# Kernel tuning notes

Hardware: AMD Instinct MI355X
Metric: run time of the kernel (lower is better)

## Reference

```python
import jax, jax.numpy as jnp
import numpy as np

N_NODES = 50000
N_EDGES = 1600000
D_IN = 192   # n_features + n_graphfea
D_HID = 128


def _gcn_conv(x, W, b, src, dst, dhis, n):
    """GCNConv returning two views.
    view1: symmetric-normalized propagation with self-loops (standard GCN).
    view2: raw neighbor sum of transformed features (to be scaled by D_inv outside).
    dhis: deg_hat^{-1/2} per node, deg_hat = in-degree + 1 (self loop).
    """
    h = x @ W + b                                      # [N, hid]
    w = dhis[src] * dhis[dst]                          # [E] edge norm
    view1 = jax.ops.segment_sum(h[src] * w[:, None], dst, num_segments=n)
    view1 = view1 + h * (dhis * dhis)[:, None]         # self-loop term
    view2 = jax.ops.segment_sum(h[src], dst, num_segments=n)
    return view1, view2


def setup_inputs() -> dict:
    key = jax.random.key(0)
    ks = jax.random.split(key, 12)
    x = jax.random.normal(ks[0], (N_NODES, D_IN), dtype=jnp.float32)
    view2 = jax.random.normal(ks[1], (N_NODES, D_IN), dtype=jnp.float32)
    edge_index = jax.random.randint(ks[2], (2, N_EDGES), 0, N_NODES, dtype=jnp.int64)
    D_inv = jax.random.uniform(ks[3], (N_NODES, 1), dtype=jnp.float32)
    def glorot(k, fan_in, fan_out):
        s = jnp.sqrt(jnp.float32(2.0 / (fan_in + fan_out)))
        return jax.random.normal(k, (fan_in, fan_out), dtype=jnp.float32) * s
    W1 = glorot(ks[4], D_IN, D_HID)
    W2 = glorot(ks[5], D_HID, D_HID)
    W3 = glorot(ks[6], D_HID, D_HID)
    W4 = glorot(ks[7], D_IN, D_HID)
    W5 = glorot(ks[8], D_HID, D_HID)
    W6 = glorot(ks[9], D_HID, D_HID)
    z = jnp.zeros((D_HID,), dtype=jnp.float32)
    return {"x": x, "view2": view2, "edge_index": edge_index, "D_inv": D_inv,
            "W1": W1, "b1": z, "W2": W2, "b2": z, "W3": W3, "b3": z,
            "W4": W4, "b4": z, "W5": W5, "b5": z, "W6": W6, "b6": z}


def reference(x, view2, edge_index, D_inv,
              W1, b1, W2, b2, W3, b3, W4, b4, W5, b5, W6, b6):
    n = x.shape[0]
    src, dst = edge_index[0], edge_index[1]
    deg = jax.ops.segment_sum(jnp.ones_like(dst, dtype=x.dtype), dst, num_segments=n)
    dhis = jax.lax.rsqrt(deg + 1.0)                    # deg_hat^{-1/2}
    relu = jax.nn.relu

    x1v1, x1v2 = _gcn_conv(x, W1, b1, src, dst, dhis, n)
    x2v1, x2v2 = _gcn_conv(view2, W4, b4, src, dst, dhis, n)
    x1 = relu(x1v1 + x2v2 * D_inv)
    x2 = relu(x2v1 + x1v2 * D_inv)

    z1v1, z1v2 = _gcn_conv(x1, W2, b2, src, dst, dhis, n)
    z2v1, z2v2 = _gcn_conv(x2, W5, b5, src, dst, dhis, n)
    z1 = relu(z1v1 + z2v2 * D_inv)
    z2 = relu(z2v1 + z1v2 * D_inv)

    v1v1, v1v2 = _gcn_conv(z1, W3, b3, src, dst, dhis, n)
    v2v1, v2v2 = _gcn_conv(z2, W6, b6, src, dst, dhis, n)
    v1 = relu(v1v1 + v2v2 * D_inv)
    v2 = relu(v2v1 + v1v2 * D_inv)

    q = jnp.concatenate([x1, z1, v1], axis=1)          # [N, 3*hid]
    p = jnp.concatenate([x2, z2, v2], axis=1)
    return q, p
```

## Files before the change

kernel.cpp:

```cpp
#include <hip/hip_runtime.h>

#define N_NODES 50000
#define N_EDGES 1600000
#define D_IN 192
#define D_HID 128

#define NSLICE 8
#define SLICE_SZ ((N_NODES + NSLICE - 1) / NSLICE)

typedef __bf16 bf16x8 __attribute__((ext_vector_type(8)));
typedef float f32x4 __attribute__((ext_vector_type(4)));

__device__ __forceinline__ unsigned short f2b(float x) {
    unsigned u = __builtin_bit_cast(unsigned, x);
    u += 0x7FFFu + ((u >> 16) & 1u);
    return (unsigned short)(u >> 16);
}
__device__ __forceinline__ float blo(unsigned u) {
    return __builtin_bit_cast(float, u << 16);
}
__device__ __forceinline__ float bhi(unsigned u) {
    return __builtin_bit_cast(float, u & 0xFFFF0000u);
}


__global__ void hist_kernel(const int* __restrict__ dst, int E,
                            int* __restrict__ cnt, int* __restrict__ rank) {
    int e = blockIdx.x * blockDim.x + threadIdx.x;
    if (e < E) rank[e] = atomicAdd(&cnt[dst[e]], 1);
}

__global__ __launch_bounds__(256) void scanA(const int* __restrict__ cnt,
                                             int* __restrict__ bsum, int n) {
    int i = blockIdx.x * 256 + threadIdx.x;
    int v = (i < n) ? cnt[i] : 0;
#pragma unroll
    for (int off = 32; off > 0; off >>= 1) v += __shfl_down(v, off);
    __shared__ int ws[4];
    if ((threadIdx.x & 63) == 0) ws[threadIdx.x >> 6] = v;
    __syncthreads();
    if (threadIdx.x == 0) bsum[blockIdx.x] = ws[0] + ws[1] + ws[2] + ws[3];
}

__global__ __launch_bounds__(256) void scanB(const int* __restrict__ bsum,
                                             int* __restrict__ boff,
                                             int* __restrict__ row_ptr, int nb, int n) {
    __shared__ int s[256];
    int tid = threadIdx.x;
    int v = (tid < nb) ? bsum[tid] : 0;
    s[tid] = v;
    __syncthreads();
    for (int off = 1; off < 256; off <<= 1) {
        int add = (tid >= off) ? s[tid - off] : 0;
        __syncthreads();
        s[tid] += add;
        __syncthreads();
    }
    if (tid < nb) boff[tid] = (tid > 0) ? s[tid - 1] : 0;
    if (tid == 0) row_ptr[n] = s[255];
}

__global__ __launch_bounds__(256) void scanC(const int* __restrict__ cnt,
                                             const int* __restrict__ boff,
                                             int* __restrict__ row_ptr,
                                             float* __restrict__ dhis, int n) {
    __shared__ int s[256];
    int tid = threadIdx.x;
    int i = blockIdx.x * 256 + tid;
    int c = (i < n) ? cnt[i] : 0;
    s[tid] = c;
    __syncthreads();
    for (int off = 1; off < 256; off <<= 1) {
        int add = (tid >= off) ? s[tid - off] : 0;
        __syncthreads();
        s[tid] += add;
        __syncthreads();
    }
    if (i < n) {
        int pre = boff[blockIdx.x] + s[tid] - c;
        row_ptr[i] = pre;
        dhis[i] = rsqrtf((float)c + 1.0f);
    }
}

__global__ __launch_bounds__(256) void fill_sliced(
        const int* __restrict__ src, const int* __restrict__ dst,
        const int* __restrict__ rank, const int* __restrict__ row_ptr,
        int* __restrict__ esrc, int E, int nchunks) {
    int slice = blockIdx.x & (NSLICE - 1);
    int chunk = blockIdx.x >> 3;
    int lo = slice * SLICE_SZ;
    int hi = lo + SLICE_SZ;
    int per = (E + nchunks - 1) / nchunks;
    int e0 = chunk * per;
    int e1 = min(e0 + per, E);
    for (int e = e0 + threadIdx.x; e < e1; e += 256) {
        int d = dst[e];
        if (d >= lo && d < hi) {
            esrc[row_ptr[d] + rank[e]] = src[e];
        }
    }
}


__global__ void prep_w(const float* __restrict__ W, unsigned short* __restrict__ Wt, int K) {
    int idx = blockIdx.x * 256 + threadIdx.x;
    if (idx < 128 * K) {
        int j = idx / K, k = idx - j * K;
        Wt[idx] = f2b(W[(size_t)k * 128 + j]);
    }
}


__global__ __launch_bounds__(256) void gemm_mfma(
        const float* __restrict__ A, int lda, int K, int Kp,
        const unsigned short* __restrict__ Wt, const float* __restrict__ bias,
        unsigned short* __restrict__ out, int M) {
    __shared__ __align__(16) unsigned short As[64 * 200];

    int tid = threadIdx.x;
    int row0 = blockIdx.x * 64;

    {
        int r = tid >> 2;
        int q = tid & 3;
        int grow = row0 + r;
        int crow = grow < M ? grow : (M - 1);
        int kq = K >> 2;
        const float* ap = A + (size_t)crow * lda + q * kq;
        unsigned short* sp = As + r * Kp + q * kq;
        for (int k = 0; k < kq; k += 4) {
            float4 v = *(const float4*)(ap + k);
            sp[k + 0] = f2b(v.x); sp[k + 1] = f2b(v.y);
            sp[k + 2] = f2b(v.z); sp[k + 3] = f2b(v.w);
        }
    }
    __syncthreads();

    int wave = tid >> 6, lane = tid & 63;
    int m = lane & 15, quad = lane >> 4;

    f32x4 acc[8];
#pragma unroll
    for (int g = 0; g < 8; ++g) acc[g] = (f32x4){0.f, 0.f, 0.f, 0.f};

    int nsteps = K >> 5;
    for (int ks = 0; ks < nsteps; ++ks) {
        int k0 = ks * 32 + quad * 8;
        bf16x8 af = *(const bf16x8*)(As + (wave * 16 + m) * Kp + k0);
#pragma unroll
        for (int g = 0; g < 8; ++g) {
            bf16x8 bfr = *(const bf16x8*)(Wt + (size_t)(g * 16 + m) * K + k0);
            acc[g] = __builtin_amdgcn_mfma_f32_16x16x32_bf16(af, bfr, acc[g], 0, 0, 0);
        }
    }

#pragma unroll
    for (int g = 0; g < 8; ++g) {
        int col = g * 16 + m;
        float bv = bias[col];
#pragma unroll
        for (int r = 0; r < 4; ++r) {
            int grow = row0 + wave * 16 + quad * 4 + r;
            if (grow < M) out[(size_t)grow * 128 + col] = f2b(acc[g][r] + bv);
        }
    }
}


__global__ __launch_bounds__(256) void agg_kernel(
        const unsigned short* __restrict__ h1b, const unsigned short* __restrict__ h2b,
        const int* __restrict__ row_ptr, const int* __restrict__ esrc,
        const float* __restrict__ dhis, const float* __restrict__ D_inv,
        float* __restrict__ out_q, float* __restrict__ out_p, int n) {
    int wave = threadIdx.x >> 6, lane = threadIdx.x & 63;
    int d = blockIdx.x * 4 + wave;
    if (d >= n) return;

    const unsigned* r1 = (const unsigned*)h1b;
    const unsigned* r2 = (const unsigned*)h2b;

    int e0 = row_ptr[d], e1 = row_ptr[d + 1];
    float a1x = 0.f, a1y = 0.f, g1x = 0.f, g1y = 0.f;
    float a2x = 0.f, a2y = 0.f, g2x = 0.f, g2y = 0.f;

    int e = e0;
    for (; e + 4 <= e1; e += 4) {
        int s0 = esrc[e], s1 = esrc[e + 1], s2 = esrc[e + 2], s3 = esrc[e + 3];
        float d0 = dhis[s0], d1 = dhis[s1], d2 = dhis[s2], d3 = dhis[s3];
        unsigned u10 = r1[(size_t)s0 * 64 + lane], u11 = r1[(size_t)s1 * 64 + lane];
        unsigned u12 = r1[(size_t)s2 * 64 + lane], u13 = r1[(size_t)s3 * 64 + lane];
        unsigned u20 = r2[(size_t)s0 * 64 + lane], u21 = r2[(size_t)s1 * 64 + lane];
        unsigned u22 = r2[(size_t)s2 * 64 + lane], u23 = r2[(size_t)s3 * 64 + lane];
        float v;
        v = blo(u10); a1x += v; g1x = fmaf(v, d0, g1x);
        v = bhi(u10); a1y += v; g1y = fmaf(v, d0, g1y);
        v = blo(u11); a1x += v; g1x = fmaf(v, d1, g1x);
        v = bhi(u11); a1y += v; g1y = fmaf(v, d1, g1y);
        v = blo(u12); a1x += v; g1x = fmaf(v, d2, g1x);
        v = bhi(u12); a1y += v; g1y = fmaf(v, d2, g1y);
        v = blo(u13); a1x += v; g1x = fmaf(v, d3, g1x);
        v = bhi(u13); a1y += v; g1y = fmaf(v, d3, g1y);
        v = blo(u20); a2x += v; g2x = fmaf(v, d0, g2x);
        v = bhi(u20); a2y += v; g2y = fmaf(v, d0, g2y);
        v = blo(u21); a2x += v; g2x = fmaf(v, d1, g2x);
        v = bhi(u21); a2y += v; g2y = fmaf(v, d1, g2y);
        v = blo(u22); a2x += v; g2x = fmaf(v, d2, g2x);
        v = bhi(u22); a2y += v; g2y = fmaf(v, d2, g2y);
        v = blo(u23); a2x += v; g2x = fmaf(v, d3, g2x);
        v = bhi(u23); a2y += v; g2y = fmaf(v, d3, g2y);
    }
    for (; e < e1; ++e) {
        int s = esrc[e];
        float ds = dhis[s];
        unsigned u1 = r1[(size_t)s * 64 + lane];
        unsigned u2 = r2[(size_t)s * 64 + lane];
        float v;
        v = blo(u1); a1x += v; g1x = fmaf(v, ds, g1x);
        v = bhi(u1); a1y += v; g1y = fmaf(v, ds, g1y);
        v = blo(u2); a2x += v; g2x = fmaf(v, ds, g2x);
        v = bhi(u2); a2y += v; g2y = fmaf(v, ds, g2y);
    }

    float dh = dhis[d];
    float di = D_inv[d];
    float dh2 = dh * dh;
    unsigned us1 = r1[(size_t)d * 64 + lane];
    unsigned us2 = r2[(size_t)d * 64 + lane];

    float o1x = fmaf(dh, g1x, fmaf(blo(us1), dh2, a2x * di));
    float o1y = fmaf(dh, g1y, fmaf(bhi(us1), dh2, a2y * di));
    float o2x = fmaf(dh, g2x, fmaf(blo(us2), dh2, a1x * di));
    float o2y = fmaf(dh, g2y, fmaf(bhi(us2), dh2, a1y * di));

    float2 oq = make_float2(fmaxf(o1x, 0.f), fmaxf(o1y, 0.f));
    float2 op = make_float2(fmaxf(o2x, 0.f), fmaxf(o2y, 0.f));
    *(float2*)(out_q + (size_t)d * 384 + lane * 2) = oq;
    *(float2*)(out_p + (size_t)d * 384 + lane * 2) = op;
}


extern "C" void kernel_launch(void* const* d_in, const int* in_sizes, int n_in,
                              void* d_out, int out_size, void* d_ws, size_t ws_size,
                              hipStream_t stream) {
    const float* x     = (const float*)d_in[0];
    const float* view2 = (const float*)d_in[1];
    const int*   eidx  = (const int*)d_in[2];
    const float* D_inv = (const float*)d_in[3];
    const float* W1 = (const float*)d_in[4];  const float* b1 = (const float*)d_in[5];
    const float* W2 = (const float*)d_in[6];  const float* b2 = (const float*)d_in[7];
    const float* W3 = (const float*)d_in[8];  const float* b3 = (const float*)d_in[9];
    const float* W4 = (const float*)d_in[10]; const float* b4 = (const float*)d_in[11];
    const float* W5 = (const float*)d_in[12]; const float* b5 = (const float*)d_in[13];
    const float* W6 = (const float*)d_in[14]; const float* b6 = (const float*)d_in[15];

    const int n = N_NODES;
    const int E = N_EDGES;
    const int* src  = eidx;
    const int* dstv = eidx + E;

    char* ws = (char*)d_ws;
    size_t off = 0;
    auto alloc = [&](size_t bytes) -> void* {
        void* p = ws + off;
        off += (bytes + 255) & ~(size_t)255;
        return p;
    };
    int*   cnt     = (int*)alloc((size_t)n * 4);
    int*   row_ptr = (int*)alloc((size_t)(n + 1) * 4);
    float* dhis    = (float*)alloc((size_t)n * 4);
    int*   rank    = (int*)alloc((size_t)E * 4);
    int*   esrc    = (int*)alloc((size_t)E * 4);
    int*   bsum    = (int*)alloc((size_t)256 * 4);
    int*   boff    = (int*)alloc((size_t)256 * 4);
    unsigned short* h1b = (unsigned short*)alloc((size_t)n * 128 * 2);
    unsigned short* h2b = (unsigned short*)alloc((size_t)n * 128 * 2);
    unsigned short* Wt1 = (unsigned short*)alloc((size_t)128 * 192 * 2);
    unsigned short* Wt4 = (unsigned short*)alloc((size_t)128 * 192 * 2);
    unsigned short* Wt2 = (unsigned short*)alloc((size_t)128 * 128 * 2);
    unsigned short* Wt3 = (unsigned short*)alloc((size_t)128 * 128 * 2);
    unsigned short* Wt5 = (unsigned short*)alloc((size_t)128 * 128 * 2);
    unsigned short* Wt6 = (unsigned short*)alloc((size_t)128 * 128 * 2);

    float* qb = (float*)d_out;
    float* pb = qb + (size_t)n * 384;

    hipMemsetAsync(cnt, 0, (size_t)n * 4, stream);
    int eblocks = (E + 255) / 256;
    int nb = (n + 255) / 256;
    hist_kernel<<<eblocks, 256, 0, stream>>>(dstv, E, cnt, rank);
    scanA<<<nb, 256, 0, stream>>>(cnt, bsum, n);
    scanB<<<1, 256, 0, stream>>>(bsum, boff, row_ptr, nb, n);
    scanC<<<nb, 256, 0, stream>>>(cnt, boff, row_ptr, dhis, n);
    int nchunks = 1024;
    fill_sliced<<<nchunks * NSLICE, 256, 0, stream>>>(src, dstv, rank, row_ptr, esrc, E, nchunks);

    prep_w<<<(128 * 192 + 255) / 256, 256, 0, stream>>>(W1, Wt1, 192);
    prep_w<<<(128 * 192 + 255) / 256, 256, 0, stream>>>(W4, Wt4, 192);
    prep_w<<<(128 * 128 + 255) / 256, 256, 0, stream>>>(W2, Wt2, 128);
    prep_w<<<(128 * 128 + 255) / 256, 256, 0, stream>>>(W3, Wt3, 128);
    prep_w<<<(128 * 128 + 255) / 256, 256, 0, stream>>>(W5, Wt5, 128);
    prep_w<<<(128 * 128 + 255) / 256, 256, 0, stream>>>(W6, Wt6, 128);

    int gblocks = (n + 63) / 64;
    int ablocks = (n + 3) / 4;

    gemm_mfma<<<gblocks, 256, 0, stream>>>(x,     D_IN, 192, 200, Wt1, b1, h1b, n);
    gemm_mfma<<<gblocks, 256, 0, stream>>>(view2, D_IN, 192, 200, Wt4, b4, h2b, n);
    agg_kernel<<<ablocks, 256, 0, stream>>>(h1b, h2b, row_ptr, esrc, dhis, D_inv, qb + 0, pb + 0, n);

    gemm_mfma<<<gblocks, 256, 0, stream>>>(qb, 384, 128, 136, Wt2, b2, h1b, n);
    gemm_mfma<<<gblocks, 256, 0, stream>>>(pb, 384, 128, 136, Wt5, b5, h2b, n);
    agg_kernel<<<ablocks, 256, 0, stream>>>(h1b, h2b, row_ptr, esrc, dhis, D_inv, qb + 128, pb + 128, n);

    gemm_mfma<<<gblocks, 256, 0, stream>>>(qb + 128, 384, 128, 136, Wt3, b3, h1b, n);
    gemm_mfma<<<gblocks, 256, 0, stream>>>(pb + 128, 384, 128, 136, Wt6, b6, h2b, n);
    agg_kernel<<<ablocks, 256, 0, stream>>>(h1b, h2b, row_ptr, esrc, dhis, D_inv, qb + 256, pb + 256, n);
}
```

Before: 852.6 us.

## Interleave both views' features and pack edge source with its norm weight

The GEMMs now write both views' bf16 features into one combined row per node, with column pairs interleaved, so the aggregation issues one 8-byte gather per edge instead of two 4-byte gathers. The CSR fill step stores the source index together with dhis[src] as an int2, which removes the dependent dhis gather in the aggregation loop. The aggregation math uses packed float2 vector ops. The GEMM output stores become strided 4-byte-apart scatters, and the edge array doubles in size.

```diff
diff --git a/kernel.cpp b/kernel.cpp
--- a/kernel.cpp
+++ b/kernel.cpp
@@ -10,6 +10,7 @@
 
 typedef __bf16 bf16x8 __attribute__((ext_vector_type(8)));
 typedef float f32x4 __attribute__((ext_vector_type(4)));
+typedef float f32x2 __attribute__((ext_vector_type(2)));
 
 __device__ __forceinline__ unsigned short f2b(float x) {
     unsigned u = __builtin_bit_cast(unsigned, x);
@@ -86,7 +87,8 @@
 __global__ __launch_bounds__(256) void fill_sliced(
         const int* __restrict__ src, const int* __restrict__ dst,
         const int* __restrict__ rank, const int* __restrict__ row_ptr,
-        int* __restrict__ esrc, int E, int nchunks) {
+        const float* __restrict__ dhis,
+        int2* __restrict__ edata, int E, int nchunks) {
     int slice = blockIdx.x & (NSLICE - 1);
     int chunk = blockIdx.x >> 3;
     int lo = slice * SLICE_SZ;
@@ -97,7 +99,9 @@
     for (int e = e0 + threadIdx.x; e < e1; e += 256) {
         int d = dst[e];
         if (d >= lo && d < hi) {
-            esrc[row_ptr[d] + rank[e]] = src[e];
+            int s = src[e];
+            edata[row_ptr[d] + rank[e]] =
+                make_int2(s, __builtin_bit_cast(int, dhis[s]));
         }
     }
 }
@@ -115,7 +119,7 @@
 __global__ __launch_bounds__(256) void gemm_mfma(
         const float* __restrict__ A, int lda, int K, int Kp,
         const unsigned short* __restrict__ Wt, const float* __restrict__ bias,
-        unsigned short* __restrict__ out, int M) {
+        unsigned short* __restrict__ out, int view, int M) {
     __shared__ __align__(16) unsigned short As[64 * 200];
 
     int tid = threadIdx.x;
@@ -159,84 +163,78 @@
     for (int g = 0; g < 8; ++g) {
         int col = g * 16 + m;
         float bv = bias[col];
+        int ci = ((col >> 1) << 2) + (view << 1) + (col & 1);
 #pragma unroll
         for (int r = 0; r < 4; ++r) {
             int grow = row0 + wave * 16 + quad * 4 + r;
-            if (grow < M) out[(size_t)grow * 128 + col] = f2b(acc[g][r] + bv);
+            if (grow < M) out[(size_t)grow * 256 + ci] = f2b(acc[g][r] + bv);
         }
     }
 }
 
 
 __global__ __launch_bounds__(256) void agg_kernel(
-        const unsigned short* __restrict__ h1b, const unsigned short* __restrict__ h2b,
-        const int* __restrict__ row_ptr, const int* __restrict__ esrc,
+        const unsigned* __restrict__ hcomb,
+        const int* __restrict__ row_ptr, const int2* __restrict__ edata,
         const float* __restrict__ dhis, const float* __restrict__ D_inv,
         float* __restrict__ out_q, float* __restrict__ out_p, int n) {
     int wave = threadIdx.x >> 6, lane = threadIdx.x & 63;
     int d = blockIdx.x * 4 + wave;
     if (d >= n) return;
 
-    const unsigned* r1 = (const unsigned*)h1b;
-    const unsigned* r2 = (const unsigned*)h2b;
-
     int e0 = row_ptr[d], e1 = row_ptr[d + 1];
-    float a1x = 0.f, a1y = 0.f, g1x = 0.f, g1y = 0.f;
-    float a2x = 0.f, a2y = 0.f, g2x = 0.f, g2y = 0.f;
+    f32x2 a1 = {0.f, 0.f}, g1 = {0.f, 0.f};
+    f32x2 a2 = {0.f, 0.f}, g2 = {0.f, 0.f};
+
+#define EDGE_BODY(u, w) {                                         \
+        f32x2 v1 = {blo((u).x), bhi((u).x)};                      \
+        f32x2 v2 = {blo((u).y), bhi((u).y)};                      \
+        f32x2 wv = {(w), (w)};                                    \
+        a1 += v1; g1 = __builtin_elementwise_fma(v1, wv, g1);     \
+        a2 += v2; g2 = __builtin_elementwise_fma(v2, wv, g2); }
 
     int e = e0;
     for (; e + 4 <= e1; e += 4) {
-        int s0 = esrc[e], s1 = esrc[e + 1], s2 = esrc[e + 2], s3 = esrc[e + 3];
-        float d0 = dhis[s0], d1 = dhis[s1], d2 = dhis[s2], d3 = dhis[s3];
-        unsigned u10 = r1[(size_t)s0 * 64 + lane], u11 = r1[(size_t)s1 * 64 + lane];
-        unsigned u12 = r1[(size_t)s2 * 64 + lane], u13 = r1[(size_t)s3 * 64 + lane];
-        unsigned u20 = r2[(size_t)s0 * 64 + lane], u21 = r2[(size_t)s1 * 64 + lane];
-        unsigned u22 = r2[(size_t)s2 * 64 + lane], u23 = r2[(size_t)s3 * 64 + lane];
-        float v;
-        v = blo(u10); a1x += v; g1x = fmaf(v, d0, g1x);
-        v = bhi(u10); a1y += v; g1y = fmaf(v, d0, g1y);
-        v = blo(u11); a1x += v; g1x = fmaf(v, d1, g1x);
-        v = bhi(u11); a1y += v; g1y = fmaf(v, d1, g1y);
-        v = blo(u12); a1x += v; g1x = fmaf(v, d2, g1x);
-        v = bhi(u12); a1y += v; g1y = fmaf(v, d2, g1y);
-        v = blo(u13); a1x += v; g1x = fmaf(v, d3, g1x);
-        v = bhi(u13); a1y += v; g1y = fmaf(v, d3, g1y);
-        v = blo(u20); a2x += v; g2x = fmaf(v, d0, g2x);
-        v = bhi(u20); a2y += v; g2y = fmaf(v, d0, g2y);
-        v = blo(u21); a2x += v; g2x = fmaf(v, d1, g2x);
-        v = bhi(u21); a2y += v; g2y = fmaf(v, d1, g2y);
-        v = blo(u22); a2x += v; g2x = fmaf(v, d2, g2x);
-        v = bhi(u22); a2y += v; g2y = fmaf(v, d2, g2y);
-        v = blo(u23); a2x += v; g2x = fmaf(v, d3, g2x);
-        v = bhi(u23); a2y += v; g2y = fmaf(v, d3, g2y);
+        int4 ea = *(const int4*)(edata + e);
+        int4 eb = *(const int4*)(edata + e + 2);
+        uint2 u0 = *((const uint2*)(hcomb + ((size_t)ea.x << 7)) + lane);
+        uint2 u1 = *((const uint2*)(hcomb + ((size_t)ea.z << 7)) + lane);
+        uint2 u2 = *((const uint2*)(hcomb + ((size_t)eb.x << 7)) + lane);
+        uint2 u3 = *((const uint2*)(hcomb + ((size_t)eb.z << 7)) + lane);
+        float w0 = __builtin_bit_cast(float, ea.y);
+        float w1 = __builtin_bit_cast(float, ea.w);
+        float w2 = __builtin_bit_cast(float, eb.y);
+        float w3 = __builtin_bit_cast(float, eb.w);
+        EDGE_BODY(u0, w0); EDGE_BODY(u1, w1);
+        EDGE_BODY(u2, w2); EDGE_BODY(u3, w3);
     }
     for (; e < e1; ++e) {
-        int s = esrc[e];
-        float ds = dhis[s];
-        unsigned u1 = r1[(size_t)s * 64 + lane];
-        unsigned u2 = r2[(size_t)s * 64 + lane];
-        float v;
-        v = blo(u1); a1x += v; g1x = fmaf(v, ds, g1x);
-        v = bhi(u1); a1y += v; g1y = fmaf(v, ds, g1y);
-        v = blo(u2); a2x += v; g2x = fmaf(v, ds, g2x);
-        v = bhi(u2); a2y += v; g2y = fmaf(v, ds, g2y);
-    }
+        int2 ed = edata[e];
+        uint2 u = *((const uint2*)(hcomb + ((size_t)ed.x << 7)) + lane);
+        float w = __builtin_bit_cast(float, ed.y);
+        EDGE_BODY(u, w);
+    }
+#undef EDGE_BODY
 
     float dh = dhis[d];
     float di = D_inv[d];
     float dh2 = dh * dh;
-    unsigned us1 = r1[(size_t)d * 64 + lane];
-    unsigned us2 = r2[(size_t)d * 64 + lane];
-
-    float o1x = fmaf(dh, g1x, fmaf(blo(us1), dh2, a2x * di));
-    float o1y = fmaf(dh, g1y, fmaf(bhi(us1), dh2, a2y * di));
-    float o2x = fmaf(dh, g2x, fmaf(blo(us2), dh2, a1x * di));
-    float o2y = fmaf(dh, g2y, fmaf(bhi(us2), dh2, a1y * di));
-
-    float2 oq = make_float2(fmaxf(o1x, 0.f), fmaxf(o1y, 0.f));
-    float2 op = make_float2(fmaxf(o2x, 0.f), fmaxf(o2y, 0.f));
-    *(float2*)(out_q + (size_t)d * 384 + lane * 2) = oq;
-    *(float2*)(out_p + (size_t)d * 384 + lane * 2) = op;
+    f32x2 dhv = {dh, dh}, dh2v = {dh2, dh2}, div = {di, di};
+
+    uint2 us = *((const uint2*)(hcomb + ((size_t)d << 7)) + lane);
+    f32x2 s1 = {blo(us.x), bhi(us.x)};
+    f32x2 s2 = {blo(us.y), bhi(us.y)};
+
+    f32x2 o1 = __builtin_elementwise_fma(g1, dhv,
+               __builtin_elementwise_fma(s1, dh2v, a2 * div));
+    f32x2 o2 = __builtin_elementwise_fma(g2, dhv,
+               __builtin_elementwise_fma(s2, dh2v, a1 * div));
+
+    f32x2 zero = {0.f, 0.f};
+    o1 = __builtin_elementwise_max(o1, zero);
+    o2 = __builtin_elementwise_max(o2, zero);
+    *(f32x2*)(out_q + (size_t)d * 384 + lane * 2) = o1;
+    *(f32x2*)(out_p + (size_t)d * 384 + lane * 2) = o2;
 }
 
 
@@ -270,11 +268,10 @@
     int*   row_ptr = (int*)alloc((size_t)(n + 1) * 4);
     float* dhis    = (float*)alloc((size_t)n * 4);
     int*   rank    = (int*)alloc((size_t)E * 4);
-    int*   esrc    = (int*)alloc((size_t)E * 4);
+    int2*  edata   = (int2*)alloc((size_t)E * 8);
     int*   bsum    = (int*)alloc((size_t)256 * 4);
     int*   boff    = (int*)alloc((size_t)256 * 4);
-    unsigned short* h1b = (unsigned short*)alloc((size_t)n * 128 * 2);
-    unsigned short* h2b = (unsigned short*)alloc((size_t)n * 128 * 2);
+    unsigned short* hcomb = (unsigned short*)alloc((size_t)n * 256 * 2);
     unsigned short* Wt1 = (unsigned short*)alloc((size_t)128 * 192 * 2);
     unsigned short* Wt4 = (unsigned short*)alloc((size_t)128 * 192 * 2);
     unsigned short* Wt2 = (unsigned short*)alloc((size_t)128 * 128 * 2);
@@ -293,7 +290,8 @@
     scanB<<<1, 256, 0, stream>>>(bsum, boff, row_ptr, nb, n);
     scanC<<<nb, 256, 0, stream>>>(cnt, boff, row_ptr, dhis, n);
     int nchunks = 1024;
-    fill_sliced<<<nchunks * NSLICE, 256, 0, stream>>>(src, dstv, rank, row_ptr, esrc, E, nchunks);
+    fill_sliced<<<nchunks * NSLICE, 256, 0, stream>>>(src, dstv, rank, row_ptr,
+                                                      dhis, edata, E, nchunks);
 
     prep_w<<<(128 * 192 + 255) / 256, 256, 0, stream>>>(W1, Wt1, 192);
     prep_w<<<(128 * 192 + 255) / 256, 256, 0, stream>>>(W4, Wt4, 192);
@@ -304,16 +302,17 @@
 
     int gblocks = (n + 63) / 64;
     int ablocks = (n + 3) / 4;
-
-    gemm_mfma<<<gblocks, 256, 0, stream>>>(x,     D_IN, 192, 200, Wt1, b1, h1b, n);
-    gemm_mfma<<<gblocks, 256, 0, stream>>>(view2, D_IN, 192, 200, Wt4, b4, h2b, n);
-    agg_kernel<<<ablocks, 256, 0, stream>>>(h1b, h2b, row_ptr, esrc, dhis, D_inv, qb + 0, pb + 0, n);
-
-    gemm_mfma<<<gblocks, 256, 0, stream>>>(qb, 384, 128, 136, Wt2, b2, h1b, n);
-    gemm_mfma<<<gblocks, 256, 0, stream>>>(pb, 384, 128, 136, Wt5, b5, h2b, n);
-    agg_kernel<<<ablocks, 256, 0, stream>>>(h1b, h2b, row_ptr, esrc, dhis, D_inv, qb + 128, pb + 128, n);
-
-    gemm_mfma<<<gblocks, 256, 0, stream>>>(qb + 128, 384, 128, 136, Wt3, b3, h1b, n);
-    gemm_mfma<<<gblocks, 256, 0, stream>>>(pb + 128, 384, 128, 136, Wt6, b6, h2b, n);
-    agg_kernel<<<ablocks, 256, 0, stream>>>(h1b, h2b, row_ptr, esrc, dhis, D_inv, qb + 256, pb + 256, n);
-}
+    const unsigned* hc = (const unsigned*)hcomb;
+
+    gemm_mfma<<<gblocks, 256, 0, stream>>>(x,     D_IN, 192, 200, Wt1, b1, hcomb, 0, n);
+    gemm_mfma<<<gblocks, 256, 0, stream>>>(view2, D_IN, 192, 200, Wt4, b4, hcomb, 1, n);
+    agg_kernel<<<ablocks, 256, 0, stream>>>(hc, row_ptr, edata, dhis, D_inv, qb + 0, pb + 0, n);
+
+    gemm_mfma<<<gblocks, 256, 0, stream>>>(qb, 384, 128, 136, Wt2, b2, hcomb, 0, n);
+    gemm_mfma<<<gblocks, 256, 0, stream>>>(pb, 384, 128, 136, Wt5, b5, hcomb, 1, n);
+    agg_kernel<<<ablocks, 256, 0, stream>>>(hc, row_ptr, edata, dhis, D_inv, qb + 128, pb + 128, n);
+
+    gemm_mfma<<<gblocks, 256, 0, stream>>>(qb + 128, 384, 128, 136, Wt3, b3, hcomb, 0, n);
+    gemm_mfma<<<gblocks, 256, 0, stream>>>(pb + 128, 384, 128, 136, Wt6, b6, hcomb, 1, n);
+    agg_kernel<<<ablocks, 256, 0, stream>>>(hc, row_ptr, edata, dhis, D_inv, qb + 256, pb + 256, n);
+}
```

Result: slower. 881.1 us (+3.3%).
